# Performance work log

Hardware: AMD Instinct MI355X
Metric: run time of the kernel (lower is better)

## Reference

```python
import jax, jax.numpy as jnp
import numpy as np

B, H, L, D = 2, 16, 2048, 64


def setup_inputs() -> dict:
    key = jax.random.key(0)
    kq, kk, kv = jax.random.split(key, 3)
    q = jax.random.normal(kq, (B, H, L, D), dtype=jnp.float32)
    k = jax.random.normal(kk, (B, H, L, D), dtype=jnp.float32)
    v = jax.random.normal(kv, (B, H, L, D), dtype=jnp.float32)
    return {"q": q, "k": k, "v": v}


def reference(q, k, v):
    use_norm = True
    seq_len = q.shape[-2]
    scale = q.shape[-1] ** (-0.5)
    q = q * scale
    # [B, H, L, L] score matrix
    attn = jnp.einsum("bhqd,bhkd->bhqk", q, k)
    # 2nd-order Taylor expansion of exp: 1 + s + 0.5*s^2
    attn = 1.0 + attn + 0.5 * attn * attn
    # causal mask (lower-triangular kept)
    causal = jnp.tril(jnp.ones((seq_len, seq_len), dtype=bool))
    attn = jnp.where(causal, attn, 0.0)
    o = jnp.einsum("bhqk,bhkd->bhqd", attn, v)
    if use_norm:
        z = attn.sum(-1)
        o = o / (z[..., None] + 1e-06)
    return o
```

## Files before the change

### kernel.cpp

```cpp
#include <hip/hip_runtime.h>
#include <hip/hip_bf16.h>

typedef __bf16    bf16x8  __attribute__((ext_vector_type(8)));
typedef __bf16    bf16x4  __attribute__((ext_vector_type(4)));
typedef _Float16  half8   __attribute__((ext_vector_type(8)));
typedef _Float16  half4   __attribute__((ext_vector_type(4)));
typedef _Float16  half2   __attribute__((ext_vector_type(2)));
typedef float     floatx4 __attribute__((ext_vector_type(4)));

constexpr int Bc  = 2;
constexpr int Hc  = 16;
constexpr int Lc  = 2048;
constexpr int Dc  = 64;
constexpr int BHn = Bc * Hc;
constexpr int BM  = 128;
constexpr int BN  = 64;
constexpr int NQT = Lc / BM;
constexpr int LDP = 72;
constexpr int BUFB = BN * LDP * 2 + Dc * LDP * 2;

static __device__ __forceinline__ half2 pack_f16(float a, float b) {
    return __builtin_bit_cast(half2, __builtin_amdgcn_cvt_pkrtz(a, b));
}

__global__ void prep(const float* __restrict__ kp, const float* __restrict__ vp,
                     __bf16* __restrict__ k16, _Float16* __restrict__ v16) {
    const int bid = blockIdx.x, tid = threadIdx.x;
    if (bid < 1024) {
        const size_t base = (size_t)bid * 4096 + tid * 4;
        #pragma unroll
        for (int rep = 0; rep < 4; ++rep) {
            const size_t i = base + rep * 1024;
            floatx4 v = *(const floatx4*)(kp + i);
            bf16x4 b;
            b[0] = (__bf16)v[0]; b[1] = (__bf16)v[1]; b[2] = (__bf16)v[2]; b[3] = (__bf16)v[3];
            *(bf16x4*)(k16 + i) = b;
        }
    } else {
        const int vb  = bid - 1024;
        const int bh  = vb >> 5, kt = vb & 31;
        const int key = kt * 64 + (tid & 63);
        const int k5  = key & 31;
        const int pcol = (key & ~31) | (((k5 >> 2) & 3) * 8 + ((k5 >> 4) & 1) * 4 + (k5 & 3));
        const int d0  = (tid >> 6) * 16;
        const float* src = vp + ((size_t)bh * Lc + key) * Dc;
        _Float16*    dst = v16 + (size_t)bh * Dc * Lc + pcol;
        #pragma unroll
        for (int i = 0; i < 16; ++i) {
            const int d = d0 + i;
            dst[(size_t)d * Lc] = (_Float16)src[d];
        }
    }
}

__global__ __launch_bounds__(256, 2)
void taylor_attn(const float* __restrict__ qp, const __bf16* __restrict__ k16,
                 const _Float16* __restrict__ v16, float* __restrict__ op)
{
    alignas(16) __shared__ unsigned char smem[2 * BUFB];

    const int tid  = threadIdx.x;
    const int wv   = tid >> 6;
    const int lane = tid & 63;
    const int lm   = lane & 15;
    const int quad = lane >> 4;

    const int cu    = (int)(blockIdx.x & 255);
    const int snd   = (int)(blockIdx.x >> 8);
    const int bh    = cu & 31;
    const int qslot = cu >> 5;
    const int qi    = snd ? qslot : (NQT - 1 - qslot);
    const int q0    = qi * BM;
    const int jmax  = 2 * qi + 1;

    const float*    qbase = qp  + ((size_t)bh * Lc + q0) * Dc;
    const __bf16*   kbase = k16 + (size_t)bh * Lc * Dc;
    const _Float16* vbase = v16 + (size_t)bh * Dc * Lc;

    const int gr = tid >> 3;
    const int gc = (tid & 7) * 8;

    bf16x8 kr[2]; half8 vr[2];
    const __bf16*   kj = kbase;
    const _Float16* vj = vbase;
    kr[0] = *(const bf16x8*)(kj + 8 * tid);
    kr[1] = *(const bf16x8*)(kj + 8 * (tid + 256));
    vr[0] = *(const half8*)(vj + (size_t)gr * Lc + gc);
    vr[1] = *(const half8*)(vj + (size_t)(gr + 32) * Lc + gc);

    {
        __bf16* Qs = (__bf16*)smem;
        const int r0 = tid >> 4, c4 = tid & 15;
        #pragma unroll
        for (int rep = 0; rep < 8; ++rep) {
            const int row = r0 + rep * 16;
            floatx4 v = *(const floatx4*)(qbase + row * Dc + c4 * 4);
            bf16x4 b;
            b[0] = (__bf16)v[0]; b[1] = (__bf16)v[1]; b[2] = (__bf16)v[2]; b[3] = (__bf16)v[3];
            *(bf16x4*)&Qs[row * LDP + c4 * 4] = b;
        }
    }
    __syncthreads();
    bf16x8 qa[2][2];
    {
        __bf16* Qs = (__bf16*)smem;
        #pragma unroll
        for (int st = 0; st < 2; ++st)
            #pragma unroll
            for (int kf = 0; kf < 2; ++kf)
                qa[st][kf] = *(const bf16x8*)&Qs[(32 * wv + 16 * st + lm) * LDP + kf * 32 + quad * 8];
    }
    __syncthreads();

    floatx4 oacc[2][4] = {};
    floatx4 zacc[2]    = {};

    const half8 ones = {(_Float16)1.f, (_Float16)1.f, (_Float16)1.f, (_Float16)1.f,
                        (_Float16)1.f, (_Float16)1.f, (_Float16)1.f, (_Float16)1.f};
    const half2 c8  = {(_Float16)0.125f, (_Float16)0.125f};
    const half2 c1  = {(_Float16)1.f,    (_Float16)1.f};
    const half2 ch  = {(_Float16)0.5f,   (_Float16)0.5f};

    for (int j = 0; j <= jmax; ++j) {
        __bf16*   Ks = (__bf16*)(smem + (j & 1) * BUFB);
        _Float16* VT = (_Float16*)(smem + (j & 1) * BUFB + BN * LDP * 2);

        *(bf16x8*)&Ks[gr * LDP + gc]        = kr[0];
        *(bf16x8*)&Ks[(gr + 32) * LDP + gc] = kr[1];
        *(half8*)&VT[gr * LDP + gc]         = vr[0];
        *(half8*)&VT[(gr + 32) * LDP + gc]  = vr[1];

        __syncthreads();

        if (j < jmax) {
            kj += BN * Dc;
            vj += BN;
            kr[0] = *(const bf16x8*)(kj + 8 * tid);
            kr[1] = *(const bf16x8*)(kj + 8 * (tid + 256));
            vr[0] = *(const half8*)(vj + (size_t)gr * Lc + gc);
            vr[1] = *(const half8*)(vj + (size_t)(gr + 32) * Lc + gc);
        }

        floatx4 sacc[2][4] = {};
        #pragma unroll
        for (int kb = 0; kb < 4; ++kb)
            #pragma unroll
            for (int kf = 0; kf < 2; ++kf) {
                bf16x8 ka = *(const bf16x8*)&Ks[(16 * kb + lm) * LDP + kf * 32 + quad * 8];
                sacc[0][kb] = __builtin_amdgcn_mfma_f32_16x16x32_bf16(ka, qa[0][kf], sacc[0][kb], 0, 0, 0);
                sacc[1][kb] = __builtin_amdgcn_mfma_f32_16x16x32_bf16(ka, qa[1][kf], sacc[1][kb], 0, 0, 0);
            }

        half8 wf[2][2];
        #pragma unroll
        for (int st = 0; st < 2; ++st) {
            const int  strip_lo = q0 + 32 * wv + 16 * st;
            const bool nm  = (j * BN + 63 > strip_lo);
            const int  thr = strip_lo + lm - j * BN;
            half2 wh[4][2];
            #pragma unroll
            for (int kb = 0; kb < 4; ++kb) {
                half2 s01 = pack_f16(sacc[st][kb][0], sacc[st][kb][1]);
                half2 s23 = pack_f16(sacc[st][kb][2], sacc[st][kb][3]);
                half2 a01 = s01 * c8 + c1;
                half2 a23 = s23 * c8 + c1;
                half2 w01 = a01 * (a01 * ch) + ch;
                half2 w23 = a23 * (a23 * ch) + ch;
                if (nm) {
                    const int i0 = 16 * kb + 4 * quad;
                    w01[0] = (i0 + 0 <= thr) ? w01[0] : (_Float16)0.f;
                    w01[1] = (i0 + 1 <= thr) ? w01[1] : (_Float16)0.f;
                    w23[0] = (i0 + 2 <= thr) ? w23[0] : (_Float16)0.f;
                    w23[1] = (i0 + 3 <= thr) ? w23[1] : (_Float16)0.f;
                }
                wh[kb][0] = w01;
                wh[kb][1] = w23;
            }
            #pragma unroll
            for (int grp = 0; grp < 2; ++grp) {
                half4 lo = __builtin_shufflevector(wh[2 * grp][0],     wh[2 * grp][1],     0, 1, 2, 3);
                half4 hi = __builtin_shufflevector(wh[2 * grp + 1][0], wh[2 * grp + 1][1], 0, 1, 2, 3);
                wf[st][grp] = __builtin_shufflevector(lo, hi, 0, 1, 2, 3, 4, 5, 6, 7);
            }
        }

        #pragma unroll
        for (int db = 0; db < 4; ++db)
            #pragma unroll
            for (int grp = 0; grp < 2; ++grp) {
                half8 va = *(const half8*)&VT[(16 * db + lm) * LDP + 32 * grp + 8 * quad];
                oacc[0][db] = __builtin_amdgcn_mfma_f32_16x16x32_f16(va, wf[0][grp], oacc[0][db], 0, 0, 0);
                oacc[1][db] = __builtin_amdgcn_mfma_f32_16x16x32_f16(va, wf[1][grp], oacc[1][db], 0, 0, 0);
            }
        #pragma unroll
        for (int grp = 0; grp < 2; ++grp) {
            zacc[0] = __builtin_amdgcn_mfma_f32_16x16x32_f16(ones, wf[0][grp], zacc[0], 0, 0, 0);
            zacc[1] = __builtin_amdgcn_mfma_f32_16x16x32_f16(ones, wf[1][grp], zacc[1], 0, 0, 0);
        }
    }

    #pragma unroll
    for (int st = 0; st < 2; ++st) {
        const float inv = 1.0f / (zacc[st][0] + 1e-6f);
        const int qrow = q0 + 32 * wv + 16 * st + lm;
        float* orow = op + ((size_t)bh * Lc + qrow) * Dc;
        #pragma unroll
        for (int db = 0; db < 4; ++db)
            #pragma unroll
            for (int r = 0; r < 4; ++r)
                orow[16 * db + 4 * quad + r] = oacc[st][db][r] * inv;
    }
}

extern "C" void kernel_launch(void* const* d_in, const int* in_sizes, int n_in,
                              void* d_out, int out_size, void* d_ws, size_t ws_size,
                              hipStream_t stream) {
    const float* q = (const float*)d_in[0];
    const float* k = (const float*)d_in[1];
    const float* v = (const float*)d_in[2];
    float* o = (float*)d_out;

    __bf16*   k16 = (__bf16*)d_ws;
    _Float16* v16 = (_Float16*)((char*)d_ws + (size_t)BHn * Lc * Dc * 2);

    prep<<<dim3(2048), dim3(256), 0, stream>>>(k, v, k16, v16);
    taylor_attn<<<dim3(NQT * BHn), dim3(256), 0, stream>>>(q, k16, v16, o);
}
```

Measured before the change: 123.5 us.

## Double key tile to 128 and use a single LDS buffer with trailing barrier

Raises the key/value tile from 64 to 128 rows, which halves the number of main-loop iterations and barriers. The double-buffered LDS area becomes a single K buffer and a single V^T buffer, with a second barrier at the end of each iteration. The causal mask now runs only on the diagonal tile. This cuts per-iteration overhead, but each thread holds twice the prefetch registers, and the extra barrier serialises LDS reuse. That may hurt occupancy or the overlap of loads with MFMA work.

```diff
diff --git a/kernel.cpp b/kernel.cpp
--- a/kernel.cpp
+++ b/kernel.cpp
@@ -14,10 +14,10 @@
 constexpr int Dc  = 64;
 constexpr int BHn = Bc * Hc;
 constexpr int BM  = 128;
-constexpr int BN  = 64;
+constexpr int BN  = 128;
 constexpr int NQT = Lc / BM;
-constexpr int LDP = 72;
-constexpr int BUFB = BN * LDP * 2 + Dc * LDP * 2;
+constexpr int LDK = 72;
+constexpr int LDV = 136;
 
 static __device__ __forceinline__ half2 pack_f16(float a, float b) {
     return __builtin_bit_cast(half2, __builtin_amdgcn_cvt_pkrtz(a, b));
@@ -57,7 +57,8 @@
 void taylor_attn(const float* __restrict__ qp, const __bf16* __restrict__ k16,
                  const _Float16* __restrict__ v16, float* __restrict__ op)
 {
-    alignas(16) __shared__ unsigned char smem[2 * BUFB];
+    __shared__ __bf16   Ks[BN * LDK];
+    __shared__ _Float16 VT[Dc * LDV];
 
     const int tid  = threadIdx.x;
     const int wv   = tid >> 6;
@@ -71,25 +72,23 @@
     const int qslot = cu >> 5;
     const int qi    = snd ? qslot : (NQT - 1 - qslot);
     const int q0    = qi * BM;
-    const int jmax  = 2 * qi + 1;
+    const int jmax  = qi;
 
     const float*    qbase = qp  + ((size_t)bh * Lc + q0) * Dc;
-    const __bf16*   kbase = k16 + (size_t)bh * Lc * Dc;
-    const _Float16* vbase = v16 + (size_t)bh * Dc * Lc;
-
-    const int gr = tid >> 3;
-    const int gc = (tid & 7) * 8;
-
-    bf16x8 kr[2]; half8 vr[2];
-    const __bf16*   kj = kbase;
-    const _Float16* vj = vbase;
-    kr[0] = *(const bf16x8*)(kj + 8 * tid);
-    kr[1] = *(const bf16x8*)(kj + 8 * (tid + 256));
-    vr[0] = *(const half8*)(vj + (size_t)gr * Lc + gc);
-    vr[1] = *(const half8*)(vj + (size_t)(gr + 32) * Lc + gc);
+    const __bf16*   kj    = k16 + (size_t)bh * Lc * Dc;
+    const _Float16* vj    = v16 + (size_t)bh * Dc * Lc;
+
+    bf16x8 kr[4]; half8 vr[4];
+    #pragma unroll
+    for (int rep = 0; rep < 4; ++rep)
+        kr[rep] = *(const bf16x8*)(kj + 8 * (tid + 256 * rep));
+    #pragma unroll
+    for (int rep = 0; rep < 4; ++rep) {
+        const int g = tid + 256 * rep;
+        vr[rep] = *(const half8*)(vj + (size_t)(g >> 4) * Lc + (g & 15) * 8);
+    }
 
     {
-        __bf16* Qs = (__bf16*)smem;
         const int r0 = tid >> 4, c4 = tid & 15;
         #pragma unroll
         for (int rep = 0; rep < 8; ++rep) {
@@ -97,19 +96,16 @@
             floatx4 v = *(const floatx4*)(qbase + row * Dc + c4 * 4);
             bf16x4 b;
             b[0] = (__bf16)v[0]; b[1] = (__bf16)v[1]; b[2] = (__bf16)v[2]; b[3] = (__bf16)v[3];
-            *(bf16x4*)&Qs[row * LDP + c4 * 4] = b;
+            *(bf16x4*)&Ks[row * LDK + c4 * 4] = b;
         }
     }
     __syncthreads();
     bf16x8 qa[2][2];
-    {
-        __bf16* Qs = (__bf16*)smem;
-        #pragma unroll
-        for (int st = 0; st < 2; ++st)
-            #pragma unroll
-            for (int kf = 0; kf < 2; ++kf)
-                qa[st][kf] = *(const bf16x8*)&Qs[(32 * wv + 16 * st + lm) * LDP + kf * 32 + quad * 8];
-    }
+    #pragma unroll
+    for (int st = 0; st < 2; ++st)
+        #pragma unroll
+        for (int kf = 0; kf < 2; ++kf)
+            qa[st][kf] = *(const bf16x8*)&Ks[(32 * wv + 16 * st + lm) * LDK + kf * 32 + quad * 8];
     __syncthreads();
 
     floatx4 oacc[2][4] = {};
@@ -122,81 +118,94 @@
     const half2 ch  = {(_Float16)0.5f,   (_Float16)0.5f};
 
     for (int j = 0; j <= jmax; ++j) {
-        __bf16*   Ks = (__bf16*)(smem + (j & 1) * BUFB);
-        _Float16* VT = (_Float16*)(smem + (j & 1) * BUFB + BN * LDP * 2);
-
-        *(bf16x8*)&Ks[gr * LDP + gc]        = kr[0];
-        *(bf16x8*)&Ks[(gr + 32) * LDP + gc] = kr[1];
-        *(half8*)&VT[gr * LDP + gc]         = vr[0];
-        *(half8*)&VT[(gr + 32) * LDP + gc]  = vr[1];
-
+        #pragma unroll
+        for (int rep = 0; rep < 4; ++rep) {
+            const int c = tid + 256 * rep;
+            *(bf16x8*)&Ks[(c >> 3) * LDK + (c & 7) * 8] = kr[rep];
+        }
+        #pragma unroll
+        for (int rep = 0; rep < 4; ++rep) {
+            const int g = tid + 256 * rep;
+            *(half8*)&VT[(g >> 4) * LDV + (g & 15) * 8] = vr[rep];
+        }
         __syncthreads();
 
         if (j < jmax) {
             kj += BN * Dc;
             vj += BN;
-            kr[0] = *(const bf16x8*)(kj + 8 * tid);
-            kr[1] = *(const bf16x8*)(kj + 8 * (tid + 256));
-            vr[0] = *(const half8*)(vj + (size_t)gr * Lc + gc);
-            vr[1] = *(const half8*)(vj + (size_t)(gr + 32) * Lc + gc);
-        }
-
-        floatx4 sacc[2][4] = {};
-        #pragma unroll
-        for (int kb = 0; kb < 4; ++kb)
-            #pragma unroll
-            for (int kf = 0; kf < 2; ++kf) {
-                bf16x8 ka = *(const bf16x8*)&Ks[(16 * kb + lm) * LDP + kf * 32 + quad * 8];
-                sacc[0][kb] = __builtin_amdgcn_mfma_f32_16x16x32_bf16(ka, qa[0][kf], sacc[0][kb], 0, 0, 0);
-                sacc[1][kb] = __builtin_amdgcn_mfma_f32_16x16x32_bf16(ka, qa[1][kf], sacc[1][kb], 0, 0, 0);
-            }
-
-        half8 wf[2][2];
-        #pragma unroll
-        for (int st = 0; st < 2; ++st) {
-            const int  strip_lo = q0 + 32 * wv + 16 * st;
-            const bool nm  = (j * BN + 63 > strip_lo);
-            const int  thr = strip_lo + lm - j * BN;
-            half2 wh[4][2];
-            #pragma unroll
-            for (int kb = 0; kb < 4; ++kb) {
-                half2 s01 = pack_f16(sacc[st][kb][0], sacc[st][kb][1]);
-                half2 s23 = pack_f16(sacc[st][kb][2], sacc[st][kb][3]);
-                half2 a01 = s01 * c8 + c1;
-                half2 a23 = s23 * c8 + c1;
-                half2 w01 = a01 * (a01 * ch) + ch;
-                half2 w23 = a23 * (a23 * ch) + ch;
-                if (nm) {
-                    const int i0 = 16 * kb + 4 * quad;
-                    w01[0] = (i0 + 0 <= thr) ? w01[0] : (_Float16)0.f;
-                    w01[1] = (i0 + 1 <= thr) ? w01[1] : (_Float16)0.f;
-                    w23[0] = (i0 + 2 <= thr) ? w23[0] : (_Float16)0.f;
-                    w23[1] = (i0 + 3 <= thr) ? w23[1] : (_Float16)0.f;
-                }
-                wh[kb][0] = w01;
-                wh[kb][1] = w23;
-            }
-            #pragma unroll
-            for (int grp = 0; grp < 2; ++grp) {
-                half4 lo = __builtin_shufflevector(wh[2 * grp][0],     wh[2 * grp][1],     0, 1, 2, 3);
-                half4 hi = __builtin_shufflevector(wh[2 * grp + 1][0], wh[2 * grp + 1][1], 0, 1, 2, 3);
-                wf[st][grp] = __builtin_shufflevector(lo, hi, 0, 1, 2, 3, 4, 5, 6, 7);
-            }
-        }
-
-        #pragma unroll
-        for (int db = 0; db < 4; ++db)
-            #pragma unroll
-            for (int grp = 0; grp < 2; ++grp) {
-                half8 va = *(const half8*)&VT[(16 * db + lm) * LDP + 32 * grp + 8 * quad];
-                oacc[0][db] = __builtin_amdgcn_mfma_f32_16x16x32_f16(va, wf[0][grp], oacc[0][db], 0, 0, 0);
-                oacc[1][db] = __builtin_amdgcn_mfma_f32_16x16x32_f16(va, wf[1][grp], oacc[1][db], 0, 0, 0);
-            }
-        #pragma unroll
-        for (int grp = 0; grp < 2; ++grp) {
-            zacc[0] = __builtin_amdgcn_mfma_f32_16x16x32_f16(ones, wf[0][grp], zacc[0], 0, 0, 0);
-            zacc[1] = __builtin_amdgcn_mfma_f32_16x16x32_f16(ones, wf[1][grp], zacc[1], 0, 0, 0);
-        }
+            #pragma unroll
+            for (int rep = 0; rep < 4; ++rep)
+                kr[rep] = *(const bf16x8*)(kj + 8 * (tid + 256 * rep));
+            #pragma unroll
+            for (int rep = 0; rep < 4; ++rep) {
+                const int g = tid + 256 * rep;
+                vr[rep] = *(const half8*)(vj + (size_t)(g >> 4) * Lc + (g & 15) * 8);
+            }
+        }
+
+        const bool nm = (j == jmax);
+        #pragma unroll
+        for (int half = 0; half < 2; ++half) {
+            floatx4 sacc[2][4] = {};
+            #pragma unroll
+            for (int kb4 = 0; kb4 < 4; ++kb4) {
+                const int kb = 4 * half + kb4;
+                #pragma unroll
+                for (int kf = 0; kf < 2; ++kf) {
+                    bf16x8 ka = *(const bf16x8*)&Ks[(16 * kb + lm) * LDK + kf * 32 + quad * 8];
+                    sacc[0][kb4] = __builtin_amdgcn_mfma_f32_16x16x32_bf16(ka, qa[0][kf], sacc[0][kb4], 0, 0, 0);
+                    sacc[1][kb4] = __builtin_amdgcn_mfma_f32_16x16x32_bf16(ka, qa[1][kf], sacc[1][kb4], 0, 0, 0);
+                }
+            }
+
+            half8 wf[2][2];
+            #pragma unroll
+            for (int st = 0; st < 2; ++st) {
+                const int strip_lo = q0 + 32 * wv + 16 * st;
+                const int thr = strip_lo + lm - j * BN;
+                half2 wh[4][2];
+                #pragma unroll
+                for (int kb4 = 0; kb4 < 4; ++kb4) {
+                    half2 s01 = pack_f16(sacc[st][kb4][0], sacc[st][kb4][1]);
+                    half2 s23 = pack_f16(sacc[st][kb4][2], sacc[st][kb4][3]);
+                    half2 a01 = s01 * c8 + c1;
+                    half2 a23 = s23 * c8 + c1;
+                    half2 w01 = a01 * (a01 * ch) + ch;
+                    half2 w23 = a23 * (a23 * ch) + ch;
+                    if (nm) {
+                        const int i0 = 16 * (4 * half + kb4) + 4 * quad;
+                        w01[0] = (i0 + 0 <= thr) ? w01[0] : (_Float16)0.f;
+                        w01[1] = (i0 + 1 <= thr) ? w01[1] : (_Float16)0.f;
+                        w23[0] = (i0 + 2 <= thr) ? w23[0] : (_Float16)0.f;
+                        w23[1] = (i0 + 3 <= thr) ? w23[1] : (_Float16)0.f;
+                    }
+                    wh[kb4][0] = w01;
+                    wh[kb4][1] = w23;
+                }
+                #pragma unroll
+                for (int g2 = 0; g2 < 2; ++g2) {
+                    half4 lo = __builtin_shufflevector(wh[2 * g2][0],     wh[2 * g2][1],     0, 1, 2, 3);
+                    half4 hi = __builtin_shufflevector(wh[2 * g2 + 1][0], wh[2 * g2 + 1][1], 0, 1, 2, 3);
+                    wf[st][g2] = __builtin_shufflevector(lo, hi, 0, 1, 2, 3, 4, 5, 6, 7);
+                }
+            }
+
+            #pragma unroll
+            for (int db = 0; db < 4; ++db)
+                #pragma unroll
+                for (int g2 = 0; g2 < 2; ++g2) {
+                    const int grp = 2 * half + g2;
+                    half8 va = *(const half8*)&VT[(16 * db + lm) * LDV + 32 * grp + 8 * quad];
+                    oacc[0][db] = __builtin_amdgcn_mfma_f32_16x16x32_f16(va, wf[0][g2], oacc[0][db], 0, 0, 0);
+                    oacc[1][db] = __builtin_amdgcn_mfma_f32_16x16x32_f16(va, wf[1][g2], oacc[1][db], 0, 0, 0);
+                }
+            #pragma unroll
+            for (int g2 = 0; g2 < 2; ++g2) {
+                zacc[0] = __builtin_amdgcn_mfma_f32_16x16x32_f16(ones, wf[0][g2], zacc[0], 0, 0, 0);
+                zacc[1] = __builtin_amdgcn_mfma_f32_16x16x32_f16(ones, wf[1][g2], zacc[1], 0, 0, 0);
+            }
+        }
+        __syncthreads();
     }
 
     #pragma unroll
```

Measured after the change: 119.2 us. -3.5%, faster.
